# Kernel optimization log

Measured on AMD Instinct MI355X. Metric: run time of the kernel, lower is better.

The kernel has to match this reference:

```python
import jax, jax.numpy as jnp
import numpy as np

NEG = -1e30  # effective -inf that stays stable in fp32 log-sum-exp
BLANK = 0


def _lse3(a, b, c):
    m = jnp.maximum(jnp.maximum(a, b), c)
    return m + jnp.log(jnp.exp(a - m) + jnp.exp(b - m) + jnp.exp(c - m))


def _ctc_loss_sum(log_probs, input_lengths, targets, target_lengths):
    # log_probs: [B, T, V] already log-softmaxed; targets: [B, S] int, blank=0
    B, T, V = log_probs.shape
    S = targets.shape[1]
    L = 2 * S + 1  # extended label seq: blank-interleaved

    ext = jnp.full((B, L), BLANK, dtype=targets.dtype)
    ext = ext.at[:, 1::2].set(targets)  # [B, L]

    # gather per-frame log-probs of extended labels: [B, T, L]
    lp_ext = jnp.take_along_axis(
        log_probs, jnp.broadcast_to(ext[:, None, :], (B, T, L)), axis=2)

    # skip transition s-2 -> s allowed iff ext[s] != blank and ext[s] != ext[s-2]
    ext_prev2 = jnp.pad(ext[:, :-2], ((0, 0), (2, 0)), constant_values=BLANK)
    can_skip = (ext != BLANK) & (ext != ext_prev2) & (jnp.arange(L)[None, :] >= 2)

    # alpha init at t=0
    alpha = jnp.full((B, L), NEG, dtype=log_probs.dtype)
    alpha = alpha.at[:, 0].set(lp_ext[:, 0, 0])
    alpha = alpha.at[:, 1].set(lp_ext[:, 0, 1])

    lp_seq = jnp.swapaxes(lp_ext, 0, 1)[1:]          # [T-1, B, L]
    valid = jnp.arange(1, T)[:, None] < input_lengths[None, :]  # [T-1, B]

    def step(a, xs):
        lp_t, v = xs  # [B, L], [B]
        a1 = jnp.pad(a[:, :-1], ((0, 0), (1, 0)), constant_values=NEG)
        a2 = jnp.pad(a[:, :-2], ((0, 0), (2, 0)), constant_values=NEG)
        a2 = jnp.where(can_skip, a2, NEG)
        new = _lse3(a, a1, a2) + lp_t
        a = jnp.where(v[:, None], new, a)  # freeze past each utterance's length
        return a, None

    alpha, _ = jax.lax.scan(step, alpha, (lp_seq, valid))

    # terminal states: last blank (2*tl) and last label (2*tl - 1)
    end = 2 * target_lengths.astype(jnp.int32)
    aT = jnp.take_along_axis(alpha, jnp.stack([end, end - 1], axis=1), axis=1)  # [B, 2]
    ll = jax.scipy.special.logsumexp(aT, axis=1)
    loss = -ll
    loss = jnp.where(loss > 1e29, 0.0, loss)  # zero_infinity=True
    return jnp.sum(loss)  # reduction='sum'


def setup_inputs() -> dict:
    B, T, V, S = 64, 1024, 512, 128
    key = jax.random.key(0)
    k1, k2, k3, k4 = jax.random.split(key, 4)
    output_tensor = jax.random.normal(k1, (B, T, V), dtype=jnp.float32)
    output_lengths = jax.random.randint(k2, (B,), T // 2, T + 1, dtype=jnp.int32)
    target_tensor = jax.random.randint(k3, (B, S), 1, V, dtype=jnp.int32)  # no blanks
    target_lengths = jax.random.randint(k4, (B,), S // 2, S + 1, dtype=jnp.int32)
    return {"output_tensor": output_tensor, "output_lengths": output_lengths,
            "target_tensor": target_tensor, "target_lengths": target_lengths}


def reference(output_tensor, output_lengths, target_tensor, target_lengths):
    log_probs = jax.nn.log_softmax(output_tensor, axis=2)
    return _ctc_loss_sum(log_probs, output_lengths, target_tensor, target_lengths)
```

## Files before the change

### kernel.cpp

```cpp
#include <hip/hip_runtime.h>
#include <cstdint>

#define T_LEN 1024
#define V_DIM 512
#define S_LEN 128
#define NEG2  (-1.0e30f)
#define CH    32
#define PREP_BLOCKS 2048
#define ROWS_PER_WAVE 8

__device__ float2 g_plab[(size_t)64 * T_LEN * 64 + 64];
__device__ float  g_pblank[(size_t)64 * T_LEN + 64];

static __device__ __forceinline__ void dma16(const void* g, void* l) {
    __builtin_amdgcn_global_load_lds(
        (const __attribute__((address_space(1))) unsigned int*)g,
        (__attribute__((address_space(3))) unsigned int*)l,
        16, 0, 0);
}

static __device__ __forceinline__ float dpp_shr1_f(float x) {
    return __int_as_float(__builtin_amdgcn_update_dpp(
        0, __float_as_int(x), 0x138, 0xF, 0xF, true));
}
static __device__ __forceinline__ int dpp_shr1_i(int x) {
    return __builtin_amdgcn_update_dpp(0, x, 0x138, 0xF, 0xF, true);
}
template <int CTRL>
static __device__ __forceinline__ float dpp_add(float x) {
    const int y = __builtin_amdgcn_update_dpp(0, __float_as_int(x), CTRL, 0xF, 0xF, true);
    return x + __int_as_float(y);
}

__global__ __launch_bounds__(256) void ctc_prep(
    const float* __restrict__ x, const int* __restrict__ lens,
    const int* __restrict__ tgts)
{
    const int lane = threadIdx.x & 63;
    const int wv0  = (int)((blockIdx.x * blockDim.x + threadIdx.x) >> 6);
    const float L2E = 1.44269504088896340736f;

    #pragma unroll
    for (int it = 0; it < ROWS_PER_WAVE; ++it) {
        const int wid = wv0 + it * 8192;
        const int b = wid >> 10;
        const int t = wid & (T_LEN - 1);
        if (t >= lens[b]) continue;

        const float* row = x + (size_t)wid * V_DIM;
        const float4 u = *(const float4*)(row + lane * 8);
        const float4 v = *(const float4*)(row + lane * 8 + 4);

        float s = exp2f(u.x * L2E) + exp2f(u.y * L2E)
                + exp2f(u.z * L2E) + exp2f(u.w * L2E)
                + exp2f(v.x * L2E) + exp2f(v.y * L2E)
                + exp2f(v.z * L2E) + exp2f(v.w * L2E);
        s = dpp_add<0x111>(s);
        s = dpp_add<0x112>(s);
        s = dpp_add<0x114>(s);
        s = dpp_add<0x118>(s);
        s = dpp_add<0x142>(s);
        s = dpp_add<0x143>(s);
        const float off =
            log2f(__int_as_float(__builtin_amdgcn_readlane(__float_as_int(s), 63)));

        if (lane == 0) g_pblank[wid] = exp2f(u.x * L2E - off);

        const int2 tg = *(const int2*)(tgts + b * S_LEN + 2 * lane);
        g_plab[(size_t)wid * 64 + lane] =
            make_float2(exp2f(row[tg.x] * L2E - off), exp2f(row[tg.y] * L2E - off));
    }
}

struct AlphaState { float a0, a1, a2, a3, a4; int C; };

static __device__ __forceinline__ void alpha_step(
    AlphaState& st, float pb, float2 lp, float cs1f, float cs3f, bool dead)
{
    const float p3 = dpp_shr1_f(st.a3);
    const int   Cp = dpp_shr1_i(st.C);
    const int   Cn = dead ? Cp : st.C;
    int e = 127 + (Cp - Cn);
    e = e < 0 ? 0 : (e > 252 ? 252 : e);
    const float adj = __int_as_float((unsigned)e << 23);
    const float p3v = p3 * adj;
    const float s01 = st.a0 + st.a1;
    const float s23 = st.a2 + st.a3;
    const float n0 = (st.a0 + p3v) * pb;
    const float n1 = fmaf(p3v, cs1f, s01) * lp.x;
    const float n2 = (st.a1 + st.a2) * pb;
    const float n3 = fmaf(st.a1, cs3f, s23) * lp.y;
    const float n4 = (st.a3 + st.a4) * pb;
    st.a0 = n0; st.a1 = n1; st.a2 = n2; st.a3 = n3; st.a4 = n4; st.C = Cn;
}

static __device__ __forceinline__ void alpha_rescale(AlphaState& st)
{
    const float mx = fmaxf(fmaxf(fmaxf(st.a0, st.a1), fmaxf(st.a2, st.a3)), st.a4);
    const int ee = (__float_as_int(mx) >> 23) & 255;
    const bool ok = (ee > 0) && (ee < 255);
    const float sc = ok ? __int_as_float((unsigned)(254 - ee) << 23) : 1.0f;
    const int dC = ok ? (ee - 127) : 0;
    st.a0 *= sc; st.a1 *= sc; st.a2 *= sc; st.a3 *= sc; st.a4 *= sc; st.C += dC;
}

__global__ __launch_bounds__(64) void ctc_alpha(
    const int* __restrict__ lens, const int* __restrict__ tgts,
    const int* __restrict__ tlens, float* __restrict__ out)
{
    __shared__ alignas(16) float lds_pbs[T_LEN];
    __shared__ float2 lds_pl[3][CH * 64];

    const int b    = blockIdx.x;
    const int lane = threadIdx.x;
    const int len  = lens[b];
    const int tl   = tlens[b];
    const int lenm1 = len - 1;

    const int tA = tgts[b * S_LEN + 2 * lane];
    const int tB = tgts[b * S_LEN + 2 * lane + 1];
    const int tPrev = __shfl_up(tB, 1);
    const bool cs1 = (lane > 0) && (tA != tPrev);
    const bool cs3 = (tB != tA);
    const float cs1f = cs1 ? 1.0f : 0.0f;
    const float cs3f = cs3 ? 1.0f : 0.0f;

    const int repOwn = ((lane > 0 && tA == tPrev) ? 1 : 0) + ((tB == tA) ? 1 : 0);
    int ps = repOwn;
    #pragma unroll
    for (int d = 1; d < 64; d <<= 1) {
        const int y = __shfl_up(ps, d);
        if (lane >= d) ps += y;
    }
    const int deadline = 2 * lane + (ps - repOwn);

    const size_t rowb = (size_t)b * T_LEN;
    const float*  __restrict__ pb_b = g_pblank + rowb;
    const float2* __restrict__ pl_b = g_plab + rowb * 64;

    #pragma unroll
    for (int j = 0; j < CH / 2; ++j)
        dma16(pl_b + (size_t)(1 + 2 * j) * 64 + lane * 2, &lds_pl[0][j * 128]);
    #pragma unroll
    for (int j = 0; j < CH / 2; ++j)
        dma16(pl_b + (size_t)(33 + 2 * j) * 64 + lane * 2, &lds_pl[1][j * 128]);

    #pragma unroll
    for (int k = 0; k < T_LEN / 64; ++k)
        lds_pbs[k * 64 + lane] = pb_b[k * 64 + lane + 1];

    AlphaState st;
    st.a0 = 0.f; st.a1 = 0.f; st.a2 = 0.f; st.a3 = 0.f; st.a4 = 0.f; st.C = 0;
    if (lane == 0) { st.a0 = pb_b[0]; st.a1 = pl_b[0].x; }

    int cur = 0;
    int t0 = 1;
    for (; t0 + CH <= len; t0 += CH) {
        __builtin_amdgcn_s_waitcnt(0x4F70);
        float4 pbq[CH / 4];
        #pragma unroll
        for (int j = 0; j < CH / 4; ++j)
            pbq[j] = *(const float4*)&lds_pbs[(t0 - 1) + 4 * j];
        const float* pbr = (const float*)pbq;
        float2 pl[CH];
        #pragma unroll
        for (int i = 0; i < CH; ++i)
            pl[i] = lds_pl[cur][i * 64 + lane];
        int fill = cur + 2; if (fill >= 3) fill -= 3;
        #pragma unroll
        for (int j = 0; j < CH / 2; ++j) {
            int r = t0 + 2 * CH + 2 * j;
            r = (r < lenm1) ? r : lenm1;
            dma16(pl_b + (size_t)r * 64 + lane * 2, &lds_pl[fill][j * 128]);
        }
        #pragma unroll
        for (int i = 0; i < CH; ++i) {
            const bool dead = (deadline >= t0 + i);
            alpha_step(st, pbr[i], pl[i], cs1f, cs3f, dead);
            if ((i & 3) == 3) alpha_rescale(st);
        }
        cur = (cur == 2) ? 0 : cur + 1;
    }
    __builtin_amdgcn_s_waitcnt(0x0F70);
    for (int i = 0; t0 + i < len; ++i) {
        const float2 plv = lds_pl[cur][i * 64 + lane];
        const float  pb  = lds_pbs[t0 + i - 1];
        const bool dead = (deadline >= t0 + i);
        alpha_step(st, pb, plv, cs1f, cs3f, dead);
        if ((i & 3) == 3) alpha_rescale(st);
    }

    const int end = 2 * tl;
    float v1, v2; int C1, C2;
    {
        int s = end;
        int lsrc = s >> 2; if (lsrc > 63) lsrc = 63;
        const int slot = s & 3;
        float cand = (slot == 0) ? st.a0 : (slot == 1) ? st.a1
                   : (slot == 2) ? st.a2 : st.a3;
        if (s == 256) cand = st.a4;
        v1 = __shfl(cand, lsrc);
        C1 = __shfl(st.C, lsrc);

        s = end - 1;
        lsrc = s >> 2;
        const int slot2 = s & 3;
        cand = (slot2 == 0) ? st.a0 : (slot2 == 1) ? st.a1
             : (slot2 == 2) ? st.a2 : st.a3;
        v2 = __shfl(cand, lsrc);
        C2 = __shfl(st.C, lsrc);
    }
    const float l1 = (v1 > 0.f) ? log2f(v1) + (float)C1 : NEG2;
    const float l2 = (v2 > 0.f) ? log2f(v2) + (float)C2 : NEG2;
    const float mM = fmaxf(l1, l2);
    const float ll2 = mM + log2f(exp2f(l1 - mM) + exp2f(l2 - mM));
    float loss = -ll2 * 0.69314718055994530942f;
    if (!(loss < 1e29f)) loss = 0.f;
    if (lane == 0) atomicAdd(out, loss);
}

extern "C" void kernel_launch(void* const* d_in, const int* in_sizes, int n_in,
                              void* d_out, int out_size, void* d_ws, size_t ws_size,
                              hipStream_t stream) {
    (void)in_sizes; (void)n_in; (void)d_ws; (void)ws_size;
    const float* x     = (const float*)d_in[0];
    const int*   lens  = (const int*)d_in[1];
    const int*   tgts  = (const int*)d_in[2];
    const int*   tlens = (const int*)d_in[3];
    float* out = (float*)d_out;

    (void)hipMemsetAsync(d_out, 0, (size_t)out_size * sizeof(float), stream);
    ctc_prep<<<PREP_BLOCKS, 256, 0, stream>>>(x, lens, tgts);
    ctc_alpha<<<64, 64, 0, stream>>>(lens, tgts, tlens, out);
}
```

Measured before the change: 264.4 us.

## Software-pipeline LDS loads in groups of eight and add lean post-deadline step path

The alpha recursion loop now double-buffers LDS reads in groups of eight timesteps, issuing the next group's loads before computing the current one, so LDS latency overlaps with the serial recurrence. Once every lane is past its deadline, a lean variant drops the per-step dead check and hoists the neighbour exponent adjustment to once per four steps. The DMA wait moves to the end of each chunk. This adds register pressure and code size from the two template instantiations, and relies on the exponent offsets staying fixed between rescales.

```diff
diff --git a/kernel.cpp b/kernel.cpp
--- a/kernel.cpp
+++ b/kernel.cpp
@@ -94,6 +94,21 @@
     st.a0 = n0; st.a1 = n1; st.a2 = n2; st.a3 = n3; st.a4 = n4; st.C = Cn;
 }
 
+static __device__ __forceinline__ void lean_step(
+    AlphaState& st, float pb, float2 lp, float cs1f, float cs3f, float adj)
+{
+    const float p3 = dpp_shr1_f(st.a3);
+    const float p3v = p3 * adj;
+    const float s01 = st.a0 + st.a1;
+    const float s23 = st.a2 + st.a3;
+    const float n0 = (st.a0 + p3v) * pb;
+    const float n1 = fmaf(p3v, cs1f, s01) * lp.x;
+    const float n2 = (st.a1 + st.a2) * pb;
+    const float n3 = fmaf(st.a1, cs3f, s23) * lp.y;
+    const float n4 = (st.a3 + st.a4) * pb;
+    st.a0 = n0; st.a1 = n1; st.a2 = n2; st.a3 = n3; st.a4 = n4;
+}
+
 static __device__ __forceinline__ void alpha_rescale(AlphaState& st)
 {
     const float mx = fmaxf(fmaxf(fmaxf(st.a0, st.a1), fmaxf(st.a2, st.a3)), st.a4);
@@ -104,12 +119,83 @@
     st.a0 *= sc; st.a1 *= sc; st.a2 *= sc; st.a3 *= sc; st.a4 *= sc; st.C += dC;
 }
 
+struct Grp { float2 v[8]; float4 pa, pb; };
+
+static __device__ __forceinline__ void loadG(
+    Grp& G, const float2* base ,
+    const float* pbbase )
+{
+    #pragma unroll
+    for (int j = 0; j < 8; ++j) G.v[j] = base[j * 64];
+    G.pa = *(const float4*)(pbbase);
+    G.pb = *(const float4*)(pbbase + 4);
+}
+
+template<bool LEAN>
+static __device__ __forceinline__ void computeG(
+    AlphaState& st, const Grp& G, float cs1f, float cs3f, int tb, int deadline)
+{
+    if (LEAN) {
+        {
+            const int Cp = dpp_shr1_i(st.C);
+            int e = 127 + (Cp - st.C);
+            e = e < 0 ? 0 : (e > 252 ? 252 : e);
+            const float adj = __int_as_float((unsigned)e << 23);
+            lean_step(st, G.pa.x, G.v[0], cs1f, cs3f, adj);
+            lean_step(st, G.pa.y, G.v[1], cs1f, cs3f, adj);
+            lean_step(st, G.pa.z, G.v[2], cs1f, cs3f, adj);
+            lean_step(st, G.pa.w, G.v[3], cs1f, cs3f, adj);
+            alpha_rescale(st);
+        }
+        {
+            const int Cp = dpp_shr1_i(st.C);
+            int e = 127 + (Cp - st.C);
+            e = e < 0 ? 0 : (e > 252 ? 252 : e);
+            const float adj = __int_as_float((unsigned)e << 23);
+            lean_step(st, G.pb.x, G.v[4], cs1f, cs3f, adj);
+            lean_step(st, G.pb.y, G.v[5], cs1f, cs3f, adj);
+            lean_step(st, G.pb.z, G.v[6], cs1f, cs3f, adj);
+            lean_step(st, G.pb.w, G.v[7], cs1f, cs3f, adj);
+            alpha_rescale(st);
+        }
+    } else {
+        alpha_step(st, G.pa.x, G.v[0], cs1f, cs3f, deadline >= tb + 0);
+        alpha_step(st, G.pa.y, G.v[1], cs1f, cs3f, deadline >= tb + 1);
+        alpha_step(st, G.pa.z, G.v[2], cs1f, cs3f, deadline >= tb + 2);
+        alpha_step(st, G.pa.w, G.v[3], cs1f, cs3f, deadline >= tb + 3);
+        alpha_rescale(st);
+        alpha_step(st, G.pb.x, G.v[4], cs1f, cs3f, deadline >= tb + 4);
+        alpha_step(st, G.pb.y, G.v[5], cs1f, cs3f, deadline >= tb + 5);
+        alpha_step(st, G.pb.z, G.v[6], cs1f, cs3f, deadline >= tb + 6);
+        alpha_step(st, G.pb.w, G.v[7], cs1f, cs3f, deadline >= tb + 7);
+        alpha_rescale(st);
+    }
+}
+
+template<bool LEAN>
+static __device__ __forceinline__ void chunk_body(
+    AlphaState& st, Grp& GA, Grp& GB,
+    const float2* plcur, const float2* plnxt, const float* pbs_t0m1,
+    float cs1f, float cs3f, int t0, int deadline)
+{
+    loadG(GB, plcur + 8 * 64,  pbs_t0m1 + 8);
+    computeG<LEAN>(st, GA, cs1f, cs3f, t0, deadline);
+    loadG(GA, plcur + 16 * 64, pbs_t0m1 + 16);
+    computeG<LEAN>(st, GB, cs1f, cs3f, t0 + 8, deadline);
+    loadG(GB, plcur + 24 * 64, pbs_t0m1 + 24);
+    computeG<LEAN>(st, GA, cs1f, cs3f, t0 + 16, deadline);
+    __builtin_amdgcn_s_waitcnt(0x4F70);
+    __builtin_amdgcn_sched_barrier(0);
+    loadG(GA, plnxt, pbs_t0m1 + 32);
+    computeG<LEAN>(st, GB, cs1f, cs3f, t0 + 24, deadline);
+}
+
 __global__ __launch_bounds__(64) void ctc_alpha(
     const int* __restrict__ lens, const int* __restrict__ tgts,
     const int* __restrict__ tlens, float* __restrict__ out)
 {
     __shared__ alignas(16) float lds_pbs[T_LEN];
-    __shared__ float2 lds_pl[3][CH * 64];
+    __shared__ alignas(16) float2 lds_pl[3][CH * 64];
 
     const int b    = blockIdx.x;
     const int lane = threadIdx.x;
@@ -133,6 +219,7 @@
         if (lane >= d) ps += y;
     }
     const int deadline = 2 * lane + (ps - repOwn);
+    const int dmax = __shfl(deadline, 63);
 
     const size_t rowb = (size_t)b * T_LEN;
     const float*  __restrict__ pb_b = g_pblank + rowb;
@@ -153,19 +240,15 @@
     st.a0 = 0.f; st.a1 = 0.f; st.a2 = 0.f; st.a3 = 0.f; st.a4 = 0.f; st.C = 0;
     if (lane == 0) { st.a0 = pb_b[0]; st.a1 = pl_b[0].x; }
 
+    __builtin_amdgcn_s_waitcnt(0x4F70);
+    __builtin_amdgcn_sched_barrier(0);
+
+    Grp GA, GB;
+    loadG(GA, &lds_pl[0][lane], &lds_pbs[0]);
+
     int cur = 0;
     int t0 = 1;
     for (; t0 + CH <= len; t0 += CH) {
-        __builtin_amdgcn_s_waitcnt(0x4F70);
-        float4 pbq[CH / 4];
-        #pragma unroll
-        for (int j = 0; j < CH / 4; ++j)
-            pbq[j] = *(const float4*)&lds_pbs[(t0 - 1) + 4 * j];
-        const float* pbr = (const float*)pbq;
-        float2 pl[CH];
-        #pragma unroll
-        for (int i = 0; i < CH; ++i)
-            pl[i] = lds_pl[cur][i * 64 + lane];
         int fill = cur + 2; if (fill >= 3) fill -= 3;
         #pragma unroll
         for (int j = 0; j < CH / 2; ++j) {
@@ -173,15 +256,17 @@
             r = (r < lenm1) ? r : lenm1;
             dma16(pl_b + (size_t)r * 64 + lane * 2, &lds_pl[fill][j * 128]);
         }
-        #pragma unroll
-        for (int i = 0; i < CH; ++i) {
-            const bool dead = (deadline >= t0 + i);
-            alpha_step(st, pbr[i], pl[i], cs1f, cs3f, dead);
-            if ((i & 3) == 3) alpha_rescale(st);
-        }
-        cur = (cur == 2) ? 0 : cur + 1;
+        int nxt = cur + 1; if (nxt >= 3) nxt -= 3;
+        if (t0 > dmax)
+            chunk_body<true>(st, GA, GB, &lds_pl[cur][lane], &lds_pl[nxt][lane],
+                             &lds_pbs[t0 - 1], cs1f, cs3f, t0, deadline);
+        else
+            chunk_body<false>(st, GA, GB, &lds_pl[cur][lane], &lds_pl[nxt][lane],
+                              &lds_pbs[t0 - 1], cs1f, cs3f, t0, deadline);
+        cur = nxt;
     }
     __builtin_amdgcn_s_waitcnt(0x0F70);
+    __builtin_amdgcn_sched_barrier(0);
     for (int i = 0; t0 + i < len; ++i) {
         const float2 plv = lds_pl[cur][i * 64 + lane];
         const float  pb  = lds_pbs[t0 + i - 1];
```

New measurement: 264.2 us. Within noise of the previous version (-0.1%).

## Prefetch label probs into registers with double-buffered groups and lean steps

Applied to the files above, without the earlier changes.

Drops the LDS triple-buffered DMA staging of per-frame label probabilities and instead loads them straight from global memory into registers in two alternating 16-frame groups, waiting on the older group only. It also adds a lean step variant, used once every lane's deadline has passed, that computes the neighbour scale adjustment once per four steps and skips the per-step dead/C update. This removes LDS round trips and per-step work from the serial recurrence, at the cost of more register pressure and reliance on vmcnt-based waits for latency hiding.

```diff
diff --git a/kernel.cpp b/kernel.cpp
--- a/kernel.cpp
+++ b/kernel.cpp
@@ -5,19 +5,11 @@
 #define V_DIM 512
 #define S_LEN 128
 #define NEG2  (-1.0e30f)
-#define CH    32
 #define PREP_BLOCKS 2048
 #define ROWS_PER_WAVE 8
 
 __device__ float2 g_plab[(size_t)64 * T_LEN * 64 + 64];
 __device__ float  g_pblank[(size_t)64 * T_LEN + 64];
-
-static __device__ __forceinline__ void dma16(const void* g, void* l) {
-    __builtin_amdgcn_global_load_lds(
-        (const __attribute__((address_space(1))) unsigned int*)g,
-        (__attribute__((address_space(3))) unsigned int*)l,
-        16, 0, 0);
-}
 
 static __device__ __forceinline__ float dpp_shr1_f(float x) {
     return __int_as_float(__builtin_amdgcn_update_dpp(
@@ -94,6 +86,21 @@
     st.a0 = n0; st.a1 = n1; st.a2 = n2; st.a3 = n3; st.a4 = n4; st.C = Cn;
 }
 
+static __device__ __forceinline__ void lean_step(
+    AlphaState& st, float pb, float2 lp, float cs1f, float cs3f, float adj)
+{
+    const float p3 = dpp_shr1_f(st.a3);
+    const float p3v = p3 * adj;
+    const float s01 = st.a0 + st.a1;
+    const float s23 = st.a2 + st.a3;
+    const float n0 = (st.a0 + p3v) * pb;
+    const float n1 = fmaf(p3v, cs1f, s01) * lp.x;
+    const float n2 = (st.a1 + st.a2) * pb;
+    const float n3 = fmaf(st.a1, cs3f, s23) * lp.y;
+    const float n4 = (st.a3 + st.a4) * pb;
+    st.a0 = n0; st.a1 = n1; st.a2 = n2; st.a3 = n3; st.a4 = n4;
+}
+
 static __device__ __forceinline__ void alpha_rescale(AlphaState& st)
 {
     const float mx = fmaxf(fmaxf(fmaxf(st.a0, st.a1), fmaxf(st.a2, st.a3)), st.a4);
@@ -104,12 +111,77 @@
     st.a0 *= sc; st.a1 *= sc; st.a2 *= sc; st.a3 *= sc; st.a4 *= sc; st.C += dC;
 }
 
+struct LGrp  { float2 v[16]; };
+struct PBGrp { float4 a, b, c, d; };
+
+static __device__ __forceinline__ float pbsel(const PBGrp& p, int i) {
+    const float4 q = (i < 4) ? p.a : (i < 8) ? p.b : (i < 12) ? p.c : p.d;
+    const int m = i & 3;
+    return m == 0 ? q.x : m == 1 ? q.y : m == 2 ? q.z : q.w;
+}
+
+static __device__ __forceinline__ void issueL(
+    LGrp& L, const float2* __restrict__ pl_b, int tb, int lenm1, int lane)
+{
+    #pragma unroll
+    for (int j = 0; j < 16; ++j) {
+        int r = tb + j; r = (r < lenm1) ? r : lenm1;
+        L.v[j] = pl_b[(size_t)r * 64 + lane];
+    }
+}
+
+static __device__ __forceinline__ void loadPB(PBGrp& P, const float* s) {
+    P.a = *(const float4*)(s);
+    P.b = *(const float4*)(s + 4);
+    P.c = *(const float4*)(s + 8);
+    P.d = *(const float4*)(s + 12);
+}
+
+template<bool LEAN>
+static __device__ __forceinline__ void computeG16(
+    AlphaState& st, const LGrp& L, const PBGrp& P,
+    float cs1f, float cs3f, int tb, int deadline)
+{
+    float adj = 1.0f;
+    #pragma unroll
+    for (int i = 0; i < 16; ++i) {
+        if (LEAN) {
+            if ((i & 3) == 0) {
+                const int Cp = dpp_shr1_i(st.C);
+                int e = 127 + (Cp - st.C);
+                e = e < 0 ? 0 : (e > 252 ? 252 : e);
+                adj = __int_as_float((unsigned)e << 23);
+            }
+            lean_step(st, pbsel(P, i), L.v[i], cs1f, cs3f, adj);
+        } else {
+            alpha_step(st, pbsel(P, i), L.v[i], cs1f, cs3f, deadline >= tb + i);
+        }
+        if ((i & 3) == 3) alpha_rescale(st);
+    }
+}
+
+static __device__ __forceinline__ void tail_steps(
+    AlphaState& st, const LGrp& L, const PBGrp& P,
+    float cs1f, float cs3f, int t0, int len, int deadline)
+{
+    #pragma unroll
+    for (int i = 0; i < 15; ++i) {
+        if (t0 + i < len) {
+            alpha_step(st, pbsel(P, i), L.v[i], cs1f, cs3f, deadline >= t0 + i);
+            if ((i & 3) == 3) alpha_rescale(st);
+        }
+    }
+}
+
+#define WAIT16() do { __builtin_amdgcn_sched_barrier(0);  \
+    __builtin_amdgcn_s_waitcnt(0x4F70);    \
+    __builtin_amdgcn_sched_barrier(0); } while (0)
+
 __global__ __launch_bounds__(64) void ctc_alpha(
     const int* __restrict__ lens, const int* __restrict__ tgts,
     const int* __restrict__ tlens, float* __restrict__ out)
 {
-    __shared__ alignas(16) float lds_pbs[T_LEN];
-    __shared__ float2 lds_pl[3][CH * 64];
+    __shared__ alignas(16) float lds_pbs[T_LEN + 16];
 
     const int b    = blockIdx.x;
     const int lane = threadIdx.x;
@@ -133,19 +205,13 @@
         if (lane >= d) ps += y;
     }
     const int deadline = 2 * lane + (ps - repOwn);
+    const int dmax = __shfl(deadline, 63);
 
     const size_t rowb = (size_t)b * T_LEN;
     const float*  __restrict__ pb_b = g_pblank + rowb;
     const float2* __restrict__ pl_b = g_plab + rowb * 64;
 
     #pragma unroll
-    for (int j = 0; j < CH / 2; ++j)
-        dma16(pl_b + (size_t)(1 + 2 * j) * 64 + lane * 2, &lds_pl[0][j * 128]);
-    #pragma unroll
-    for (int j = 0; j < CH / 2; ++j)
-        dma16(pl_b + (size_t)(33 + 2 * j) * 64 + lane * 2, &lds_pl[1][j * 128]);
-
-    #pragma unroll
     for (int k = 0; k < T_LEN / 64; ++k)
         lds_pbs[k * 64 + lane] = pb_b[k * 64 + lane + 1];
 
@@ -153,41 +219,38 @@
     st.a0 = 0.f; st.a1 = 0.f; st.a2 = 0.f; st.a3 = 0.f; st.a4 = 0.f; st.C = 0;
     if (lane == 0) { st.a0 = pb_b[0]; st.a1 = pl_b[0].x; }
 
-    int cur = 0;
+    LGrp LA, LB; PBGrp PA, PB_;
+    issueL(LA, pl_b, 1, lenm1, lane);
+    loadPB(PA, &lds_pbs[0]);
+
     int t0 = 1;
-    for (; t0 + CH <= len; t0 += CH) {
-        __builtin_amdgcn_s_waitcnt(0x4F70);
-        float4 pbq[CH / 4];
-        #pragma unroll
-        for (int j = 0; j < CH / 4; ++j)
-            pbq[j] = *(const float4*)&lds_pbs[(t0 - 1) + 4 * j];
-        const float* pbr = (const float*)pbq;
-        float2 pl[CH];
-        #pragma unroll
-        for (int i = 0; i < CH; ++i)
-            pl[i] = lds_pl[cur][i * 64 + lane];
-        int fill = cur + 2; if (fill >= 3) fill -= 3;
-        #pragma unroll
-        for (int j = 0; j < CH / 2; ++j) {
-            int r = t0 + 2 * CH + 2 * j;
-            r = (r < lenm1) ? r : lenm1;
-            dma16(pl_b + (size_t)r * 64 + lane * 2, &lds_pl[fill][j * 128]);
-        }
-        #pragma unroll
-        for (int i = 0; i < CH; ++i) {
-            const bool dead = (deadline >= t0 + i);
-            alpha_step(st, pbr[i], pl[i], cs1f, cs3f, dead);
-            if ((i & 3) == 3) alpha_rescale(st);
-        }
-        cur = (cur == 2) ? 0 : cur + 1;
-    }
-    __builtin_amdgcn_s_waitcnt(0x0F70);
-    for (int i = 0; t0 + i < len; ++i) {
-        const float2 plv = lds_pl[cur][i * 64 + lane];
-        const float  pb  = lds_pbs[t0 + i - 1];
-        const bool dead = (deadline >= t0 + i);
-        alpha_step(st, pb, plv, cs1f, cs3f, dead);
-        if ((i & 3) == 3) alpha_rescale(st);
+    for (; t0 + 32 <= len; t0 += 32) {
+        issueL(LB, pl_b, t0 + 16, lenm1, lane);
+        loadPB(PB_, &lds_pbs[t0 + 15]);
+        WAIT16();
+        if (t0 > dmax) computeG16<true >(st, LA, PA, cs1f, cs3f, t0, deadline);
+        else           computeG16<false>(st, LA, PA, cs1f, cs3f, t0, deadline);
+
+        issueL(LA, pl_b, t0 + 32, lenm1, lane);
+        loadPB(PA, &lds_pbs[t0 + 31]);
+        WAIT16();
+        if (t0 + 16 > dmax) computeG16<true >(st, LB, PB_, cs1f, cs3f, t0 + 16, deadline);
+        else                computeG16<false>(st, LB, PB_, cs1f, cs3f, t0 + 16, deadline);
+    }
+    if (t0 + 16 <= len) {
+        issueL(LB, pl_b, t0 + 16, lenm1, lane);
+        loadPB(PB_, &lds_pbs[t0 + 15]);
+        WAIT16();
+        if (t0 > dmax) computeG16<true >(st, LA, PA, cs1f, cs3f, t0, deadline);
+        else           computeG16<false>(st, LA, PA, cs1f, cs3f, t0, deadline);
+        t0 += 16;
+        __builtin_amdgcn_s_waitcnt(0x0F70);
+        __builtin_amdgcn_sched_barrier(0);
+        tail_steps(st, LB, PB_, cs1f, cs3f, t0, len, deadline);
+    } else {
+        __builtin_amdgcn_s_waitcnt(0x0F70);
+        __builtin_amdgcn_sched_barrier(0);
+        tail_steps(st, LA, PA, cs1f, cs3f, t0, len, deadline);
     }
 
     const int end = 2 * tl;
```

Result: faster. 258.9 us (-2.1%).
